# Kernel optimization log

Hardware: AMD Instinct MI355X
Metric: run time of the kernel (lower is better)

## Reference

```python
import jax, jax.numpy as jnp
import numpy as np

B, S, H, D = 2, 512, 32, 128
T = 2048          # max_seq_len (KV cache length)
DM = H * D        # 4096
ROPE_BASE = 10000.0


def setup_inputs() -> dict:
    key = jax.random.key(0)
    ks = jax.random.split(key, 5)
    x = jax.random.normal(ks[0], (B, S, DM), dtype=jnp.float32)
    wqkv = jax.random.normal(ks[1], (3 * DM, DM), dtype=jnp.float32) * 0.02
    wo = jax.random.normal(ks[2], (DM, DM), dtype=jnp.float32) * 0.02
    k_cache = jax.random.normal(ks[3], (B, H, T, D), dtype=jnp.float32)
    v_cache = jax.random.normal(ks[4], (B, H, T, D), dtype=jnp.float32)
    batch_idx = jnp.arange(B, dtype=jnp.int32)
    # prefill chunk written at positions T-S .. T-1
    input_pos = jnp.broadcast_to(jnp.arange(T - S, T, dtype=jnp.int32), (B, S))
    return {"x": x, "wqkv": wqkv, "wo": wo, "k_cache": k_cache,
            "v_cache": v_cache, "batch_idx": batch_idx, "input_pos": input_pos}


def _rope(x, cos, sin):
    # x: [B,S,H,D]; cos/sin: [B,S,D/2]
    xs = x.reshape(*x.shape[:-1], D // 2, 2)
    x0, x1 = xs[..., 0], xs[..., 1]
    c = cos[:, :, None, :]
    s = sin[:, :, None, :]
    out = jnp.stack([x0 * c - x1 * s, x1 * c + x0 * s], axis=-1)
    return out.reshape(x.shape)


def reference(x, wqkv, wo, k_cache, v_cache, batch_idx, input_pos):
    # fused QKV projection (torch Linear: y = x @ W^T)
    qkv = jnp.einsum('bsd,ed->bse', x, wqkv)
    q, k, v = jnp.split(qkv, 3, axis=-1)
    q = q.reshape(B, S, H, D)
    k = k.reshape(B, S, H, D)
    v = v.reshape(B, S, H, D)

    # RoPE at positions input_pos
    inv_freq = 1.0 / (ROPE_BASE ** (jnp.arange(0, D, 2, dtype=jnp.float32) / D))
    ang = input_pos.astype(jnp.float32)[..., None] * inv_freq  # [B,S,D/2]
    cos, sin = jnp.cos(ang), jnp.sin(ang)
    q = _rope(q, cos, sin)
    k = _rope(k, cos, sin)

    # scatter new k/v into caches at [batch_idx, :, input_pos]
    k_cache = k_cache.at[batch_idx[:, None], :, input_pos].set(k)
    v_cache = v_cache.at[batch_idx[:, None], :, input_pos].set(v)

    # causal block-mask over cache positions: kv_pos <= input_pos[q]
    q_bh = q.transpose(0, 2, 1, 3)  # [B,H,S,D]
    scale = 1.0 / jnp.sqrt(jnp.float32(D))
    scores = jnp.einsum('bhsd,bhtd->bhst', q_bh, k_cache) * scale
    kv_pos = jnp.arange(T, dtype=jnp.int32)
    mask = kv_pos[None, None, None, :] <= input_pos[:, None, :, None]  # [B,1,S,T]
    scores = jnp.where(mask, scores, jnp.float32(-1e30))
    attn = jax.nn.softmax(scores, axis=-1)
    y = jnp.einsum('bhst,bhtd->bhsd', attn, v_cache)
    y = y.transpose(0, 2, 1, 3).reshape(B, S, DM)
    return jnp.einsum('bsd,ed->bse', y, wo)
```

## Files before the change

### kernel.cpp

```cpp
#include <hip/hip_runtime.h>
#include <hip/hip_bf16.h>

#define NB 2
#define NS 512
#define NH 32
#define ND 128
#define NT 2048
#define NDM 4096
#define NE 12288

typedef __attribute__((ext_vector_type(4))) float f32x4;
typedef __attribute__((ext_vector_type(8))) short s16x8;
typedef unsigned int u32;

__device__ __forceinline__ short f2bs(float x) {
  unsigned int u = __float_as_uint(x);
  u += 0x7fffu + ((u >> 16) & 1u);
  return (short)(u >> 16);
}
__device__ __forceinline__ float bs2f(short s) {
  return __uint_as_float(((unsigned int)(unsigned short)s) << 16);
}
__device__ __forceinline__ s16x8 cvt8(float4 a, float4 b) {
  s16x8 o;
  o[0] = f2bs(a.x); o[1] = f2bs(a.y); o[2] = f2bs(a.z); o[3] = f2bs(a.w);
  o[4] = f2bs(b.x); o[5] = f2bs(b.y); o[6] = f2bs(b.z); o[7] = f2bs(b.w);
  return o;
}
__device__ __forceinline__ void gl16(const short* g, short* l) {
  __builtin_amdgcn_global_load_lds(
      (const __attribute__((address_space(1))) u32*)g,
      (__attribute__((address_space(3))) u32*)l, 16, 0, 0);
}

__global__ void f2b_kernel(const float* __restrict__ src, short* __restrict__ dst) {
  const size_t i = ((size_t)blockIdx.x * 256 + threadIdx.x) * 8;
  const float4* s = (const float4*)(src + i);
  *(s16x8*)(dst + i) = cvt8(s[0], s[1]);
}

__global__ __launch_bounds__(512, 2) void gemm8p(
    const short* __restrict__ A, const short* __restrict__ B,
    short* __restrict__ C, int M, int N, int K)
{
  __shared__ short ldsA[4 * 4096];
  __shared__ short ldsB[4 * 12288];

  const int tid = threadIdx.x;
  const int l   = tid & 63;
  const int w   = tid >> 6;
  const int wm  = w >> 2, wn = w & 3;
  const int m0  = blockIdx.y * 128, n0 = blockIdx.x * 384;
  const int nhalf = (K / 32) * 2;

  auto STAGE = [&](int s) {
    const int op    = s & 1;
    const int sigma = s >> 1;
    const int slot  = sigma & 3;
    const int k0    = sigma * 32;
    if (op == 0) {
      short* region = ldsA + slot * 4096;
      const int o    = tid * 16;
      const int line = o >> 7;
      const int off  = (o & 127) ^ ((line & 7) << 4);
      const int r    = (line << 1) | (off >> 6);
      const int cb   = off & 63;
      gl16(A + (size_t)(m0 + r) * K + k0 + (cb >> 1), region + (o >> 1));
    } else {
      short* region = ldsB + slot * 12288;
      #pragma unroll
      for (int c = 0; c < 3; ++c) {
        const int o    = c * 8192 + tid * 16;
        const int line = o >> 7;
        const int off  = (o & 127) ^ ((line & 7) << 4);
        const int r    = (line << 1) | (off >> 6);
        const int cb   = off & 63;
        gl16(B + (size_t)(n0 + r) * K + k0 + (cb >> 1), region + (o >> 1));
      }
    }
  };

  const int fcb = (l >> 4) << 4;
  auto FRAGA = [&](int slot, int r) -> s16x8 {
    const int line = r >> 1;
    const int off  = (((r & 1) << 6) | fcb) ^ ((line & 7) << 4);
    return *(const s16x8*)((const char*)(ldsA + slot * 4096) + (line << 7) + off);
  };
  auto FRAGB = [&](int slot, int r) -> s16x8 {
    const int line = r >> 1;
    const int off  = (((r & 1) << 6) | fcb) ^ ((line & 7) << 4);
    return *(const s16x8*)((const char*)(ldsB + slot * 12288) + (line << 7) + off);
  };

  f32x4 acc[4][6] = {};

  for (int s = 0; s < 6; ++s) STAGE(s);
  asm volatile("s_waitcnt vmcnt(4)" ::: "memory");
  __builtin_amdgcn_s_barrier();

  const int ktiles = K / 64;
  for (int j = 0; j < ktiles; ++j) {
    s16x8 bfr[6];
    #pragma unroll
    for (int q = 0; q < 4; ++q) {
      const int kk = q >> 1, mh = q & 1;
      const int slot = (2 * j + kk) & 3;
      s16x8 af[2];
      #pragma unroll
      for (int i = 0; i < 2; ++i)
        af[i] = FRAGA(slot, wm * 64 + (mh * 2 + i) * 16 + (l & 15));
      if (mh == 0) {
        #pragma unroll
        for (int i = 0; i < 6; ++i)
          bfr[i] = FRAGB(slot, wn * 96 + i * 16 + (l & 15));
      }
      const int s = 4 * j + q + 6;
      if (s < nhalf) STAGE(s);
      __builtin_amdgcn_s_barrier();
      __builtin_amdgcn_s_setprio(1);
      #pragma unroll
      for (int i = 0; i < 2; ++i)
        #pragma unroll
        for (int nf = 0; nf < 6; ++nf)
          acc[mh * 2 + i][nf] = __builtin_amdgcn_mfma_f32_16x16x32_bf16(
              af[i], bfr[nf], acc[mh * 2 + i][nf], 0, 0, 0);
      __builtin_amdgcn_s_setprio(0);
      if (q == 3) {
        if (j < ktiles - 2)       asm volatile("s_waitcnt vmcnt(4)" ::: "memory");
        else if (j == ktiles - 2) asm volatile("s_waitcnt vmcnt(0)" ::: "memory");
      }
      __builtin_amdgcn_s_barrier();
    }
  }

  #pragma unroll
  for (int mf = 0; mf < 4; ++mf) {
    const int r0 = m0 + wm * 64 + mf * 16 + (l >> 4) * 4;
    #pragma unroll
    for (int nf = 0; nf < 6; ++nf) {
      const int cc = n0 + wn * 96 + nf * 16 + (l & 15);
      #pragma unroll
      for (int jj = 0; jj < 4; ++jj)
        C[(size_t)(r0 + jj) * N + cc] = f2bs(acc[mf][nf][jj]);
    }
  }
}

template<bool C_BF16>
__global__ __launch_bounds__(256) void gemm_bt(
    const short* __restrict__ A, const short* __restrict__ B,
    void* __restrict__ Cp, int M, int N, int K)
{
  __shared__ short As[128 * 32];
  __shared__ short Bs[128 * 32];

  const int tid  = threadIdx.x;
  const int lane = tid & 63;
  const int w    = tid >> 6;
  const int wm = (w >> 1) * 64, wn = (w & 1) * 64;
  const int m0 = blockIdx.y * 128, n0 = blockIdx.x * 128;
  const int lr = lane & 15, lko = (lane >> 4) * 8;
  const int srow = lane >> 2, scol = (lane & 3) * 8;

  const short* ga = A + (size_t)(m0 + w * 32 + srow) * K + scol;
  const short* gb = B + (size_t)(n0 + w * 32 + srow) * K + scol;
  short* la = &As[(w * 32 + srow) * 32 + scol];
  short* lb = &Bs[(w * 32 + srow) * 32 + scol];
  const size_t rstep = (size_t)16 * K;

  f32x4 acc[4][4] = {};
  const int ktiles = K / 32;
  for (int kt = 0; kt < ktiles; ++kt) {
    const int ko = kt * 32;
    gl16(ga + ko,         la);
    gl16(ga + rstep + ko, la + 16 * 32);
    gl16(gb + ko,         lb);
    gl16(gb + rstep + ko, lb + 16 * 32);
    __syncthreads();

    s16x8 af[4], bf[4];
    #pragma unroll
    for (int i = 0; i < 4; ++i) {
      af[i] = *(const s16x8*)&As[(wm + i * 16 + lr) * 32 + lko];
      bf[i] = *(const s16x8*)&Bs[(wn + i * 16 + lr) * 32 + lko];
    }
    #pragma unroll
    for (int mi = 0; mi < 4; ++mi)
      #pragma unroll
      for (int ni = 0; ni < 4; ++ni)
        acc[mi][ni] = __builtin_amdgcn_mfma_f32_16x16x32_bf16(
            af[mi], bf[ni], acc[mi][ni], 0, 0, 0);
    __syncthreads();
  }

  #pragma unroll
  for (int mi = 0; mi < 4; ++mi) {
    const int r0 = m0 + wm + mi * 16 + (lane >> 4) * 4;
    #pragma unroll
    for (int ni = 0; ni < 4; ++ni) {
      const int c = n0 + wn + ni * 16 + lr;
      const f32x4 v = acc[mi][ni];
      #pragma unroll
      for (int j = 0; j < 4; ++j) {
        if constexpr (C_BF16)
          ((short*)Cp)[(size_t)(r0 + j) * N + c] = f2bs(v[j]);
        else
          ((float*)Cp)[(size_t)(r0 + j) * N + c] = v[j];
      }
    }
  }
}

template<bool A_BF16, bool C_BF16>
__global__ __launch_bounds__(256, 2) void gemm_nt(
    const void* __restrict__ Ap, const float* __restrict__ Bp,
    void* __restrict__ Cp, int M, int N, int K)
{
  constexpr int LP = 40;
  __shared__ short As[2][128][LP];
  __shared__ short Bs[2][128][LP];

  const int tid  = threadIdx.x;
  const int lane = tid & 63;
  const int wv   = tid >> 6;
  const int wm   = (wv >> 1) * 64, wn = (wv & 1) * 64;
  const int m0   = blockIdx.y * 128, n0 = blockIdx.x * 128;
  const int srow = tid >> 1, scol = (tid & 1) * 16;
  const int lr   = lane & 15, lko = (lane >> 4) * 8;

  const float* Af = (const float*)Ap;
  const short* Ab = (const short*)Ap;
  const size_t aOff = (size_t)(m0 + srow) * K + scol;
  const size_t bOff = (size_t)(n0 + srow) * K + scol;

  f32x4 acc[4][4] = {};

  if constexpr (A_BF16) {
    const s16x8* s = (const s16x8*)(Ab + aOff);
    *(s16x8*)&As[0][srow][scol]     = s[0];
    *(s16x8*)&As[0][srow][scol + 8] = s[1];
  } else {
    const float4* s = (const float4*)(Af + aOff);
    *(s16x8*)&As[0][srow][scol]     = cvt8(s[0], s[1]);
    *(s16x8*)&As[0][srow][scol + 8] = cvt8(s[2], s[3]);
  }
  {
    const float4* s = (const float4*)(Bp + bOff);
    *(s16x8*)&Bs[0][srow][scol]     = cvt8(s[0], s[1]);
    *(s16x8*)&Bs[0][srow][scol + 8] = cvt8(s[2], s[3]);
  }
  __syncthreads();

  const int ktiles = K / 32;
  for (int kt = 0; kt < ktiles; ++kt) {
    const int cur = kt & 1;
    const bool has = (kt + 1) < ktiles;
    float4 pa0, pa1, pa2, pa3, pb0, pb1, pb2, pb3;
    s16x8 qa0, qa1;
    if (has) {
      const int k1 = (kt + 1) * 32;
      if constexpr (A_BF16) {
        const s16x8* s = (const s16x8*)(Ab + aOff + k1);
        qa0 = s[0]; qa1 = s[1];
      } else {
        const float4* s = (const float4*)(Af + aOff + k1);
        pa0 = s[0]; pa1 = s[1]; pa2 = s[2]; pa3 = s[3];
      }
      const float4* s = (const float4*)(Bp + bOff + k1);
      pb0 = s[0]; pb1 = s[1]; pb2 = s[2]; pb3 = s[3];
    }
    s16x8 af[4], bf[4];
    #pragma unroll
    for (int i = 0; i < 4; ++i) {
      af[i] = *(const s16x8*)&As[cur][wm + i * 16 + lr][lko];
      bf[i] = *(const s16x8*)&Bs[cur][wn + i * 16 + lr][lko];
    }
    #pragma unroll
    for (int mi = 0; mi < 4; ++mi)
      #pragma unroll
      for (int ni = 0; ni < 4; ++ni)
        acc[mi][ni] = __builtin_amdgcn_mfma_f32_16x16x32_bf16(
            af[mi], bf[ni], acc[mi][ni], 0, 0, 0);
    if (has) {
      const int nxt = cur ^ 1;
      if constexpr (A_BF16) {
        *(s16x8*)&As[nxt][srow][scol]     = qa0;
        *(s16x8*)&As[nxt][srow][scol + 8] = qa1;
      } else {
        *(s16x8*)&As[nxt][srow][scol]     = cvt8(pa0, pa1);
        *(s16x8*)&As[nxt][srow][scol + 8] = cvt8(pa2, pa3);
      }
      *(s16x8*)&Bs[nxt][srow][scol]     = cvt8(pb0, pb1);
      *(s16x8*)&Bs[nxt][srow][scol + 8] = cvt8(pb2, pb3);
    }
    __syncthreads();
  }

  #pragma unroll
  for (int mi = 0; mi < 4; ++mi) {
    const int r0 = m0 + wm + mi * 16 + (lane >> 4) * 4;
    #pragma unroll
    for (int ni = 0; ni < 4; ++ni) {
      const int c = n0 + wn + ni * 16 + lr;
      const f32x4 v = acc[mi][ni];
      #pragma unroll
      for (int j = 0; j < 4; ++j) {
        if constexpr (C_BF16)
          ((short*)Cp)[(size_t)(r0 + j) * N + c] = f2bs(v[j]);
        else
          ((float*)Cp)[(size_t)(r0 + j) * N + c] = v[j];
      }
    }
  }
}

__global__ void copyk_kernel(const float* __restrict__ src, short* __restrict__ dst) {
  const size_t i = ((size_t)blockIdx.x * 256 + threadIdx.x) * 8;
  const float4* s = (const float4*)(src + i);
  *(s16x8*)(dst + i) = cvt8(s[0], s[1]);
}

__global__ __launch_bounds__(256) void vtrans_kernel(
    const float* __restrict__ vc, short* __restrict__ VT)
{
  __shared__ float tile[64][68];
  const int tid = threadIdx.x;
  const size_t bh = blockIdx.z;
  const int tt = blockIdx.x * 64;
  const int dd = blockIdx.y * 64;
  const int row = tid >> 2, c0 = (tid & 3) * 16;
  const float* src = vc + (bh * NT + tt + row) * ND + dd + c0;
  #pragma unroll
  for (int j = 0; j < 4; ++j)
    *(float4*)&tile[row][c0 + j * 4] = *(const float4*)(src + j * 4);
  __syncthreads();
  short tmp[16];
  #pragma unroll
  for (int i = 0; i < 16; ++i) tmp[i] = f2bs(tile[c0 + i][row]);
  short* dst = VT + (bh * ND + dd + row) * NT + tt + c0;
  *(s16x8*)dst       = *(s16x8*)&tmp[0];
  *(s16x8*)(dst + 8) = *(s16x8*)&tmp[8];
}

__global__ __launch_bounds__(256) void rope_kernel(
    const short* __restrict__ qkv, const int* __restrict__ ipos,
    const int* __restrict__ bidx, short* __restrict__ Qr,
    short* __restrict__ Kf, short* __restrict__ VT)
{
  const int bs = blockIdx.x;
  const int b = bs >> 9, s = bs & 511;
  const int tid = threadIdx.x;
  const int h = tid >> 3, r = tid & 7;
  const int pos = ipos[bs];
  const int bi = bidx[b];
  const short* base = qkv + (size_t)bs * NE + h * ND + r * 16;
  const s16x8 q0 = *(const s16x8*)(base);
  const s16x8 q1 = *(const s16x8*)(base + 8);
  const s16x8 k0 = *(const s16x8*)(base + NDM);
  const s16x8 k1 = *(const s16x8*)(base + NDM + 8);
  const s16x8 v0 = *(const s16x8*)(base + 2 * NDM);
  const s16x8 v1 = *(const s16x8*)(base + 2 * NDM + 8);
  const float scale = 0.08838834764831845f;
  s16x8 qo0, qo1, ko0, ko1;
  #pragma unroll
  for (int i = 0; i < 8; ++i) {
    const int d2 = r * 8 + i;
    const float invf = expf(-0.14391156831f * (float)d2);
    const float ang = (float)pos * invf;
    float sn, cs;
    sincosf(ang, &sn, &cs);
    float x0, x1, y0, y1;
    if (i < 4) {
      x0 = bs2f(q0[2 * i]); x1 = bs2f(q0[2 * i + 1]);
      y0 = bs2f(k0[2 * i]); y1 = bs2f(k0[2 * i + 1]);
    } else {
      x0 = bs2f(q1[2 * i - 8]); x1 = bs2f(q1[2 * i - 7]);
      y0 = bs2f(k1[2 * i - 8]); y1 = bs2f(k1[2 * i - 7]);
    }
    const short oq0 = f2bs((x0 * cs - x1 * sn) * scale);
    const short oq1 = f2bs((x1 * cs + x0 * sn) * scale);
    const short ok0 = f2bs(y0 * cs - y1 * sn);
    const short ok1 = f2bs(y1 * cs + y0 * sn);
    if (i < 4) { qo0[2*i]=oq0; qo0[2*i+1]=oq1; ko0[2*i]=ok0; ko0[2*i+1]=ok1; }
    else       { qo1[2*i-8]=oq0; qo1[2*i-7]=oq1; ko1[2*i-8]=ok0; ko1[2*i-7]=ok1; }
  }
  short* qdst = Qr + (((size_t)b * NH + h) * NS + s) * ND + r * 16;
  *(s16x8*)qdst = qo0; *(s16x8*)(qdst + 8) = qo1;
  short* kdst = Kf + (((size_t)bi * NH + h) * NT + pos) * ND + r * 16;
  *(s16x8*)kdst = ko0; *(s16x8*)(kdst + 8) = ko1;
  short* vdst = VT + (((size_t)bi * NH + h) * ND + r * 16) * NT + pos;
  #pragma unroll
  for (int i = 0; i < 16; ++i) {
    const short vv = (i < 8) ? v0[i] : v1[i - 8];
    vdst[(size_t)i * NT] = vv;
  }
}

__global__ __launch_bounds__(256, 2) void attn_kernel(
    const short* __restrict__ Q, const short* __restrict__ Kf,
    const short* __restrict__ VT, const int* __restrict__ ipos,
    short* __restrict__ Y)
{
  __shared__ short Ks[64][136];
  __shared__ short Vs[128][72];
  __shared__ short Ps[128][72];
  __shared__ int pos_sh[128];
  __shared__ int maxpos_sh;

  const int tid = threadIdx.x;
  const int lane = tid & 63;
  const int w = tid >> 6;
  const int s0 = blockIdx.x * 128;
  const int h = blockIdx.y;
  const int b = blockIdx.z;
  const int lr = lane & 15, lg = lane >> 4, lko = lg * 8;

  if (tid < 128) pos_sh[tid] = ipos[b * NS + s0 + tid];
  __syncthreads();
  if (tid == 0) {
    int m = 0;
    for (int i = 0; i < 128; ++i) m = (pos_sh[i] > m) ? pos_sh[i] : m;
    maxpos_sh = m;
  }
  __syncthreads();
  const int maxpos = maxpos_sh;

  const size_t bh = (size_t)b * NH + h;
  const short* Qp = Q + (bh * NS + s0 + w * 32) * ND;
  s16x8 qf[2][4];
  #pragma unroll
  for (int mi = 0; mi < 2; ++mi)
    #pragma unroll
    for (int kc = 0; kc < 4; ++kc)
      qf[mi][kc] = *(const s16x8*)(Qp + (size_t)(mi * 16 + lr) * ND + kc * 32 + lko);

  int prow[2][4];
  float mrun[2][4], lrun[2][4];
  #pragma unroll
  for (int mi = 0; mi < 2; ++mi)
    #pragma unroll
    for (int j = 0; j < 4; ++j) {
      prow[mi][j] = pos_sh[w * 32 + mi * 16 + lg * 4 + j];
      mrun[mi][j] = -1e30f;
      lrun[mi][j] = 0.f;
    }
  f32x4 yac[2][8] = {};

  const short* Kbase = Kf + bh * NT * ND;
  const short* Vbase = VT + bh * ND * NT;
  const int krow = tid >> 2, kc0 = (tid & 3) * 32;
  const int vrow = tid >> 1, vc0 = (tid & 1) * 32;
  const int ntl = maxpos / 64 + 1;

  for (int t = 0; t < ntl; ++t) {
    const int t0 = t * 64;
    {
      const short* src = Kbase + (size_t)(t0 + krow) * ND + kc0;
      #pragma unroll
      for (int j = 0; j < 4; ++j)
        *(s16x8*)&Ks[krow][kc0 + j * 8] = *(const s16x8*)(src + j * 8);
      const short* vsrc = Vbase + (size_t)vrow * NT + t0 + vc0;
      #pragma unroll
      for (int j = 0; j < 4; ++j)
        *(s16x8*)&Vs[vrow][vc0 + j * 8] = *(const s16x8*)(vsrc + j * 8);
    }
    __syncthreads();

    f32x4 sac[2][4] = {};
    #pragma unroll
    for (int kc = 0; kc < 4; ++kc) {
      s16x8 kfr[4];
      #pragma unroll
      for (int ni = 0; ni < 4; ++ni)
        kfr[ni] = *(const s16x8*)&Ks[ni * 16 + lr][kc * 32 + lko];
      #pragma unroll
      for (int mi = 0; mi < 2; ++mi)
        #pragma unroll
        for (int ni = 0; ni < 4; ++ni)
          sac[mi][ni] = __builtin_amdgcn_mfma_f32_16x16x32_bf16(
              qf[mi][kc], kfr[ni], sac[mi][ni], 0, 0, 0);
    }

    #pragma unroll
    for (int mi = 0; mi < 2; ++mi) {
      float alpha[4];
      #pragma unroll
      for (int j = 0; j < 4; ++j) {
        const int rp = prow[mi][j];
        float mv = -1e30f;
        #pragma unroll
        for (int ni = 0; ni < 4; ++ni) {
          float sv = sac[mi][ni][j];
          if (t0 + ni * 16 + lr > rp) sv = -1e30f;
          sac[mi][ni][j] = sv;
          mv = fmaxf(mv, sv);
        }
        #pragma unroll
        for (int off = 1; off < 16; off <<= 1)
          mv = fmaxf(mv, __shfl_xor(mv, off, 64));
        const float mo = mrun[mi][j];
        const float mn = fmaxf(mo, mv);
        const float a = __expf(mo - mn);
        mrun[mi][j] = mn;
        float rs = 0.f;
        #pragma unroll
        for (int ni = 0; ni < 4; ++ni) {
          const float p = __expf(sac[mi][ni][j] - mn);
          sac[mi][ni][j] = p;
          rs += p;
        }
        #pragma unroll
        for (int off = 1; off < 16; off <<= 1)
          rs += __shfl_xor(rs, off, 64);
        lrun[mi][j] = lrun[mi][j] * a + rs;
        alpha[j] = a;
      }
      #pragma unroll
      for (int nn = 0; nn < 8; ++nn)
        #pragma unroll
        for (int j = 0; j < 4; ++j)
          yac[mi][nn][j] *= alpha[j];
      #pragma unroll
      for (int ni = 0; ni < 4; ++ni)
        #pragma unroll
        for (int j = 0; j < 4; ++j)
          Ps[w * 32 + mi * 16 + lg * 4 + j][ni * 16 + lr] = f2bs(sac[mi][ni][j]);
    }
    __syncthreads();

    #pragma unroll
    for (int kc = 0; kc < 2; ++kc) {
      s16x8 vf[8];
      #pragma unroll
      for (int nn = 0; nn < 8; ++nn)
        vf[nn] = *(const s16x8*)&Vs[nn * 16 + lr][kc * 32 + lko];
      #pragma unroll
      for (int mi = 0; mi < 2; ++mi) {
        const s16x8 pf = *(const s16x8*)&Ps[w * 32 + mi * 16 + lr][kc * 32 + lko];
        #pragma unroll
        for (int nn = 0; nn < 8; ++nn)
          yac[mi][nn] = __builtin_amdgcn_mfma_f32_16x16x32_bf16(
              pf, vf[nn], yac[mi][nn], 0, 0, 0);
      }
    }
    __syncthreads();
  }

  #pragma unroll
  for (int mi = 0; mi < 2; ++mi)
    #pragma unroll
    for (int j = 0; j < 4; ++j) {
      const float inv = 1.0f / lrun[mi][j];
      const int srow = s0 + w * 32 + mi * 16 + lg * 4 + j;
      short* yp = Y + ((size_t)b * NS + srow) * NDM + h * ND;
      #pragma unroll
      for (int nn = 0; nn < 8; ++nn)
        yp[nn * 16 + lr] = f2bs(yac[mi][nn][j] * inv);
    }
}

extern "C" void kernel_launch(void* const* d_in, const int* in_sizes, int n_in,
                              void* d_out, int out_size, void* d_ws, size_t ws_size,
                              hipStream_t stream)
{
  (void)in_sizes; (void)n_in; (void)out_size;
  const float* x    = (const float*)d_in[0];
  const float* wqkv = (const float*)d_in[1];
  const float* wo   = (const float*)d_in[2];
  const float* kc   = (const float*)d_in[3];
  const float* vc   = (const float*)d_in[4];
  const int*   bidx = (const int*)d_in[5];
  const int*   ipos = (const int*)d_in[6];
  float* out = (float*)d_out;

  char* ws = (char*)d_ws;
  short* qkv = (short*)(ws);
  short* Qr  = (short*)(ws + 25165824ull);
  short* Kf  = (short*)(ws + 33554432ull);
  short* VT  = (short*)(ws + 67108864ull);
  short* Y   = qkv;
  short* xb  = Qr;
  short* wb  = (short*)(ws + 100663296ull);

  const size_t WS_NEEDED = 201326592ull;

  if (ws_size >= WS_NEEDED) {
    f2b_kernel<<<dim3(2048),  256, 0, stream>>>(x, xb);
    f2b_kernel<<<dim3(24576), 256, 0, stream>>>(wqkv, wb);
    gemm8p<<<dim3(NE / 384, (NB * NS) / 128), 512, 0, stream>>>(
        xb, wb, qkv, NB * NS, NE, NDM);
    copyk_kernel<<<dim3(8192), 256, 0, stream>>>(kc, Kf);
    vtrans_kernel<<<dim3(NT / 64, ND / 64, NB * NH), 256, 0, stream>>>(vc, VT);
    rope_kernel<<<dim3(NB * NS), 256, 0, stream>>>(qkv, ipos, bidx, Qr, Kf, VT);
    attn_kernel<<<dim3(NS / 128, NH, NB), 256, 0, stream>>>(Qr, Kf, VT, ipos, Y);
    f2b_kernel<<<dim3(8192), 256, 0, stream>>>(wo, wb);
    gemm_bt<false><<<dim3(NDM / 128, (NB * NS) / 128), 256, 0, stream>>>(
        Y, wb, out, NB * NS, NDM, NDM);
  } else {
    gemm_nt<false, true><<<dim3(NE / 128, (NB * NS) / 128), 256, 0, stream>>>(
        x, wqkv, qkv, NB * NS, NE, NDM);
    copyk_kernel<<<dim3(8192), 256, 0, stream>>>(kc, Kf);
    vtrans_kernel<<<dim3(NT / 64, ND / 64, NB * NH), 256, 0, stream>>>(vc, VT);
    rope_kernel<<<dim3(NB * NS), 256, 0, stream>>>(qkv, ipos, bidx, Qr, Kf, VT);
    attn_kernel<<<dim3(NS / 128, NH, NB), 256, 0, stream>>>(Qr, Kf, VT, ipos, Y);
    gemm_nt<true, false><<<dim3(NDM / 128, (NB * NS) / 128), 256, 0, stream>>>(
        Y, wo, out, NB * NS, NDM, NDM);
  }
}
```

Before: 460.1 us.

## Prefetch next K/V tile into registers and skip masking on full tiles

The attention kernel now loads the next K/V tile from global memory into registers while computing on the current tile, then writes them to LDS after the PV MMAs. This overlaps global load latency with compute. It also skips the causal mask comparison when the whole tile lies below the warp's minimum position. The mid-loop block barrier is replaced by a per-wave LDS waitcnt, since each wave only reads its own P rows. The cost is higher register pressure, which could lower occupancy.

```diff
diff --git a/kernel.cpp b/kernel.cpp
--- a/kernel.cpp
+++ b/kernel.cpp
@@ -424,6 +424,7 @@
   }
   __syncthreads();
   const int maxpos = maxpos_sh;
+  const int wmin = pos_sh[w * 32];
 
   const size_t bh = (size_t)b * NH + h;
   const short* Qp = Q + (bh * NS + s0 + w * 32) * ND;
@@ -452,19 +453,31 @@
   const int vrow = tid >> 1, vc0 = (tid & 1) * 32;
   const int ntl = maxpos / 64 + 1;
 
+  {
+    const short* src = Kbase + (size_t)krow * ND + kc0;
+    #pragma unroll
+    for (int j = 0; j < 4; ++j)
+      *(s16x8*)&Ks[krow][kc0 + j * 8] = *(const s16x8*)(src + j * 8);
+    const short* vsrc = Vbase + (size_t)vrow * NT + vc0;
+    #pragma unroll
+    for (int j = 0; j < 4; ++j)
+      *(s16x8*)&Vs[vrow][vc0 + j * 8] = *(const s16x8*)(vsrc + j * 8);
+  }
+  __syncthreads();
+
   for (int t = 0; t < ntl; ++t) {
     const int t0 = t * 64;
-    {
-      const short* src = Kbase + (size_t)(t0 + krow) * ND + kc0;
-      #pragma unroll
-      for (int j = 0; j < 4; ++j)
-        *(s16x8*)&Ks[krow][kc0 + j * 8] = *(const s16x8*)(src + j * 8);
-      const short* vsrc = Vbase + (size_t)vrow * NT + t0 + vc0;
-      #pragma unroll
-      for (int j = 0; j < 4; ++j)
-        *(s16x8*)&Vs[vrow][vc0 + j * 8] = *(const s16x8*)(vsrc + j * 8);
-    }
-    __syncthreads();
+    const bool hasnext = (t + 1) < ntl;
+
+    s16x8 kreg[4], vreg[4];
+    if (hasnext) {
+      const short* src = Kbase + (size_t)(t0 + 64 + krow) * ND + kc0;
+      #pragma unroll
+      for (int j = 0; j < 4; ++j) kreg[j] = *(const s16x8*)(src + j * 8);
+      const short* vsrc = Vbase + (size_t)vrow * NT + t0 + 64 + vc0;
+      #pragma unroll
+      for (int j = 0; j < 4; ++j) vreg[j] = *(const s16x8*)(vsrc + j * 8);
+    }
 
     f32x4 sac[2][4] = {};
     #pragma unroll
@@ -481,19 +494,25 @@
               qf[mi][kc], kfr[ni], sac[mi][ni], 0, 0, 0);
     }
 
+    const bool fulltile = (t0 + 63) <= wmin;
     #pragma unroll
     for (int mi = 0; mi < 2; ++mi) {
       float alpha[4];
       #pragma unroll
       for (int j = 0; j < 4; ++j) {
-        const int rp = prow[mi][j];
         float mv = -1e30f;
-        #pragma unroll
-        for (int ni = 0; ni < 4; ++ni) {
-          float sv = sac[mi][ni][j];
-          if (t0 + ni * 16 + lr > rp) sv = -1e30f;
-          sac[mi][ni][j] = sv;
-          mv = fmaxf(mv, sv);
+        if (fulltile) {
+          #pragma unroll
+          for (int ni = 0; ni < 4; ++ni) mv = fmaxf(mv, sac[mi][ni][j]);
+        } else {
+          const int rp = prow[mi][j];
+          #pragma unroll
+          for (int ni = 0; ni < 4; ++ni) {
+            float sv = sac[mi][ni][j];
+            if (t0 + ni * 16 + lr > rp) sv = -1e30f;
+            sac[mi][ni][j] = sv;
+            mv = fmaxf(mv, sv);
+          }
         }
         #pragma unroll
         for (int off = 1; off < 16; off <<= 1)
@@ -526,7 +545,7 @@
         for (int j = 0; j < 4; ++j)
           Ps[w * 32 + mi * 16 + lg * 4 + j][ni * 16 + lr] = f2bs(sac[mi][ni][j]);
     }
-    __syncthreads();
+    asm volatile("s_waitcnt lgkmcnt(0)" ::: "memory");
 
     #pragma unroll
     for (int kc = 0; kc < 2; ++kc) {
@@ -542,6 +561,16 @@
           yac[mi][nn] = __builtin_amdgcn_mfma_f32_16x16x32_bf16(
               pf, vf[nn], yac[mi][nn], 0, 0, 0);
       }
+    }
+    __syncthreads();
+
+    if (hasnext) {
+      #pragma unroll
+      for (int j = 0; j < 4; ++j)
+        *(s16x8*)&Ks[krow][kc0 + j * 8] = kreg[j];
+      #pragma unroll
+      for (int j = 0; j < 4; ++j)
+        *(s16x8*)&Vs[vrow][vc0 + j * 8] = vreg[j];
     }
     __syncthreads();
   }
```

After: 493.4 us. 7.2% more time.
